# Optimization experiments

Hardware: AMD Instinct MI355X
Metric: run time of the kernel (lower is better)

The kernel has to match this reference:

```python
import jax, jax.numpy as jnp
import numpy as np

TEMPERATURE = 0.07
BALANCE = 1.0


def _l2norm(x, eps=1e-12):
    return x / jnp.maximum(jnp.linalg.norm(x, axis=1, keepdims=True), eps)


def setup_inputs() -> dict:
    key = jax.random.key(0)
    k1, k2 = jax.random.split(key)
    B, K, D = 32768, 8192, 384
    features = _l2norm(jax.random.normal(k1, (B, D), dtype=jnp.float32))
    centroids = jax.random.normal(k2, (K, D), dtype=jnp.float32)
    return {"features": features, "centroids": centroids}


def reference(features, centroids):
    # centroids: [K, D] learnable; features: [B, D] sampled batch (L2-normalized)
    c = _l2norm(centroids)
    # chunked matmul + exp + row-max in source == single fused GEMM+exp+max here
    prod_exp = jnp.exp(jnp.matmul(features, c.T) / TEMPERATURE)  # [B, K]
    pos_k = jnp.argmax(prod_exp, axis=1)                          # [B] int
    prod_exp_pos = jnp.max(prod_exp, axis=1)                      # [B]
    # centroid-centroid similarity; first operand is detached in source
    cent_exp = jnp.exp(jnp.matmul(jax.lax.stop_gradient(c), c.T) / TEMPERATURE)  # [K, K]
    cent_sum = jnp.sum(cent_exp, axis=0)                          # [K]
    J = jnp.log(prod_exp_pos) - jnp.log(prod_exp_pos + cent_sum[pos_k] * BALANCE)
    return -jnp.mean(J)
```

## Files before the change

### kernel.cpp

```cpp
#include <hip/hip_runtime.h>
#include <math.h>

constexpr int B = 32768;
constexpr int K = 8192;
constexpr int D = 384;
constexpr float INV_T = 1.0f / 0.07f;

constexpr int TILE_B = 24 * 64 * 16;

typedef int    int8v    __attribute__((ext_vector_type(8)));
typedef float  floatx16 __attribute__((ext_vector_type(16)));

__global__ __launch_bounds__(64) void normalize_k(const float* __restrict__ cent,
                                                  unsigned char* __restrict__ cbs) {
    const int row = blockIdx.x, lane = threadIdx.x;
    const float* src = cent + (size_t)row * D;
    float4 x = {0.f, 0.f, 0.f, 0.f}, y = {0.f, 0.f, 0.f, 0.f};
    if (lane < 48) {
        x = *(const float4*)(src + lane * 8);
        y = *(const float4*)(src + lane * 8 + 4);
    }
    float ss = x.x * x.x + x.y * x.y + x.z * x.z + x.w * x.w
             + y.x * y.x + y.y * y.y + y.z * y.z + y.w * y.w;
#pragma unroll
    for (int off = 32; off > 0; off >>= 1) ss += __shfl_down(ss, off, 64);
    ss = __shfl(ss, 0, 64);
    const float inv = 1.0f / fmaxf(sqrtf(ss), 1e-12f);
    if (lane < 48) {
        int w0 = __builtin_amdgcn_cvt_pk_fp8_f32(x.x * inv, x.y * inv, 0, false);
        w0 = __builtin_amdgcn_cvt_pk_fp8_f32(x.z * inv, x.w * inv, w0, true);
        int w1 = __builtin_amdgcn_cvt_pk_fp8_f32(y.x * inv, y.y * inv, 0, false);
        w1 = __builtin_amdgcn_cvt_pk_fp8_f32(y.z * inv, y.w * inv, w1, true);
        char* dst = (char*)cbs + (size_t)(row >> 6) * TILE_B
                  + ((size_t)(lane >> 1) * 64 + (row & 63)) * 16 + (lane & 1) * 8;
        *(int2*)dst = make_int2(w0, w1);
    }
}

__device__ __forceinline__ void stage_tile_async(const char* __restrict__ gtile,
                                                 char* __restrict__ bs,
                                                 int wave, int lane) {
    const char* g = gtile + wave * 6144 + lane * 16;
    char* l = bs + wave * 6144;
#pragma unroll
    for (int i = 0; i < 6; ++i) {
        __builtin_amdgcn_global_load_lds(
            (const __attribute__((address_space(1))) unsigned int*)(g + i * 1024),
            (__attribute__((address_space(3))) unsigned int*)(l + i * 1024),
            16, 0, 0);
    }
}

__device__ __forceinline__ int8v read_frag(const char* base, int t, int half) {
    const uint4 b0 = *(const uint4*)(base + (4 * t + 2 * half) * 1024);
    const uint4 b1 = *(const uint4*)(base + (4 * t + 2 * half + 1) * 1024);
    int8v f;
    f[0] = b0.x; f[1] = b0.y; f[2] = b0.z; f[3] = b0.w;
    f[4] = b1.x; f[5] = b1.y; f[6] = b1.z; f[7] = b1.w;
    return f;
}

__global__ __launch_bounds__(256, 3) void centsum_k(const unsigned char* __restrict__ cbs,
                                                    float* __restrict__ cent_sum) {
    __shared__ char bs[2][TILE_B];
    const int tid = threadIdx.x, lane = tid & 63, wave = tid >> 6;
    const int wm = wave >> 1, wn = wave & 1;
    const int l31 = lane & 31, half = lane >> 5;

    int8v afr[6];
    const char* abase = (const char*)cbs + (size_t)blockIdx.x * TILE_B
                      + (wm * 32 + l31) * 16;
#pragma unroll
    for (int t = 0; t < 6; ++t) afr[t] = read_frag(abase, t, half);

    float rs[16];
#pragma unroll
    for (int r = 0; r < 16; ++r) rs[r] = 0.f;

    const int ct0 = (blockIdx.x & 7) * 8;
    auto tile_of = [&](int it) { return blockIdx.y * 64 + ((ct0 + it) & 63); };

    stage_tile_async((const char*)cbs + (size_t)tile_of(0) * TILE_B, bs[0], wave, lane);
    int cur = 0;
    for (int it = 0; it < 64; ++it) {
        __syncthreads();
        if (it + 1 < 64)
            stage_tile_async((const char*)cbs + (size_t)tile_of(it + 1) * TILE_B,
                             bs[cur ^ 1], wave, lane);
        floatx16 acc;
#pragma unroll
        for (int r = 0; r < 16; ++r) acc[r] = 0.f;
        const char* bbase = bs[cur] + (wn * 32 + l31) * 16;
#pragma unroll
        for (int t = 0; t < 6; ++t) {
            const int8v bfr = read_frag(bbase, t, half);
            acc = __builtin_amdgcn_mfma_scale_f32_32x32x64_f8f6f4(
                      afr[t], bfr, acc, 0, 0, 0, 127, 0, 127);
        }
#pragma unroll
        for (int r = 0; r < 16; ++r) rs[r] += __expf(acc[r] * INV_T);
        cur ^= 1;
    }

#pragma unroll
    for (int r = 0; r < 16; ++r) {
        float s = rs[r];
#pragma unroll
        for (int off = 1; off < 32; off <<= 1) s += __shfl_xor(s, off, 64);
        if (l31 == 0) {
            const int rowl = (r & 3) + 8 * (r >> 2) + 4 * half;
            atomicAdd(&cent_sum[blockIdx.x * 64 + wm * 32 + rowl], s);
        }
    }
}

__global__ __launch_bounds__(256, 3) void rowmax_k(const float* __restrict__ f,
                                                   const unsigned char* __restrict__ cbs,
                                                   float* __restrict__ row_max,
                                                   int* __restrict__ row_arg) {
    __shared__ char bs[2][TILE_B];
    const int tid = threadIdx.x, lane = tid & 63, wave = tid >> 6;
    const int wm = wave >> 1, wn = wave & 1;
    const int l31 = lane & 31, half = lane >> 5;

    int8v afr[6];
    const float* arow = f + ((size_t)blockIdx.x * 64 + wm * 32 + l31) * D;
#pragma unroll
    for (int t = 0; t < 6; ++t) {
        const float* p = arow + t * 64 + half * 32;
        int8v a;
#pragma unroll
        for (int q = 0; q < 8; ++q) {
            const float4 v = *(const float4*)(p + q * 4);
            int w = __builtin_amdgcn_cvt_pk_fp8_f32(v.x, v.y, 0, false);
            w = __builtin_amdgcn_cvt_pk_fp8_f32(v.z, v.w, w, true);
            a[q] = w;
        }
        afr[t] = a;
    }

    float bestv[16];
    int   besti[16];
#pragma unroll
    for (int r = 0; r < 16; ++r) { bestv[r] = -INFINITY; besti[r] = 0; }

    const int ct0 = (blockIdx.x & 7) * 16;
    auto tile_of = [&](int it) { return (ct0 + it) & (K / 64 - 1); };

    stage_tile_async((const char*)cbs + (size_t)tile_of(0) * TILE_B, bs[0], wave, lane);
    int cur = 0;
    for (int it = 0; it < K / 64; ++it) {
        __syncthreads();
        if (it + 1 < K / 64)
            stage_tile_async((const char*)cbs + (size_t)tile_of(it + 1) * TILE_B,
                             bs[cur ^ 1], wave, lane);
        floatx16 acc;
#pragma unroll
        for (int r = 0; r < 16; ++r) acc[r] = 0.f;
        const char* bbase = bs[cur] + (wn * 32 + l31) * 16;
#pragma unroll
        for (int t = 0; t < 6; ++t) {
            const int8v bfr = read_frag(bbase, t, half);
            acc = __builtin_amdgcn_mfma_scale_f32_32x32x64_f8f6f4(
                      afr[t], bfr, acc, 0, 0, 0, 127, 0, 127);
        }
        const int curCol = tile_of(it) * 64 + wn * 32 + l31;
#pragma unroll
        for (int r = 0; r < 16; ++r) {
            const float v = acc[r];
            if (v > bestv[r]) { bestv[r] = v; besti[r] = curCol; }
        }
        cur ^= 1;
    }

#pragma unroll
    for (int r = 0; r < 16; ++r) {
        float v = bestv[r]; int ix = besti[r];
#pragma unroll
        for (int off = 1; off < 32; off <<= 1) {
            const float ov = __shfl_xor(v, off, 64);
            const int   oi = __shfl_xor(ix, off, 64);
            if (ov > v || (ov == v && oi < ix)) { v = ov; ix = oi; }
        }
        bestv[r] = v; besti[r] = ix;
    }

    __syncthreads();
    float* rv = (float*)bs;
    int*   ri = (int*)bs + 128;
    if (l31 == 0) {
#pragma unroll
        for (int r = 0; r < 16; ++r) {
            const int rowl = wm * 32 + (r & 3) + 8 * (r >> 2) + 4 * half;
            rv[rowl * 2 + wn] = bestv[r];
            ri[rowl * 2 + wn] = besti[r];
        }
    }
    __syncthreads();
    if (tid < 64) {
        const float v0 = rv[tid * 2], v1 = rv[tid * 2 + 1];
        const int   i0 = ri[tid * 2], i1 = ri[tid * 2 + 1];
        const bool take1 = (v1 > v0) || (v1 == v0 && i1 < i0);
        row_max[blockIdx.x * 64 + tid] = take1 ? v1 : v0;
        row_arg[blockIdx.x * 64 + tid] = take1 ? i1 : i0;
    }
}

__global__ __launch_bounds__(256) void loss_k(const float* __restrict__ row_max,
                                              const int* __restrict__ row_arg,
                                              const float* __restrict__ cent_sum,
                                              float* __restrict__ out) {
    __shared__ float red[256];
    const int tid = threadIdx.x;
    float s = 0.f;
    for (int b = blockIdx.x * 256 + tid; b < B; b += gridDim.x * 256) {
        const float m = row_max[b];
        const float cs = cent_sum[row_arg[b]];
        s += log1pf(cs * expf(-m * INV_T));
    }
    red[tid] = s;
    __syncthreads();
    for (int off = 128; off > 0; off >>= 1) {
        if (tid < off) red[tid] += red[tid + off];
        __syncthreads();
    }
    if (tid == 0) atomicAdd(out, red[0] / (float)B);
}

extern "C" void kernel_launch(void* const* d_in, const int* in_sizes, int n_in,
                              void* d_out, int out_size, void* d_ws, size_t ws_size,
                              hipStream_t stream) {
    const float* features  = (const float*)d_in[0];
    const float* centroids = (const float*)d_in[1];
    float* out = (float*)d_out;

    char* ws = (char*)d_ws;
    unsigned char* cbs = (unsigned char*)ws;
    float* cent_sum = (float*)(ws + (size_t)(K / 64) * TILE_B);
    float* row_max  = cent_sum + K;
    int*   row_arg  = (int*)(row_max + B);

    hipMemsetAsync(cent_sum, 0, K * sizeof(float), stream);
    hipMemsetAsync(out, 0, sizeof(float), stream);
    normalize_k<<<K, 64, 0, stream>>>(centroids, cbs);
    centsum_k<<<dim3(K / 64, 2), 256, 0, stream>>>(cbs, cent_sum);
    rowmax_k<<<B / 64, 256, 0, stream>>>(features, cbs, row_max, row_arg);
    loss_k<<<64, 256, 0, stream>>>(row_max, row_arg, cent_sum, out);
}
```

Measured before the change: 278.6 us.

## Double per-wave row tile and split column range across blocks in GEMM kernels

After: 235.4 us. 15.5% less time.

```diff
diff --git a/kernel.cpp b/kernel.cpp
--- a/kernel.cpp
+++ b/kernel.cpp
@@ -60,163 +60,193 @@
     return f;
 }
 
-__global__ __launch_bounds__(256, 3) void centsum_k(const unsigned char* __restrict__ cbs,
+__global__ __launch_bounds__(256, 2) void centsum_k(const unsigned char* __restrict__ cbs,
                                                     float* __restrict__ cent_sum) {
     __shared__ char bs[2][TILE_B];
     const int tid = threadIdx.x, lane = tid & 63, wave = tid >> 6;
     const int wm = wave >> 1, wn = wave & 1;
     const int l31 = lane & 31, half = lane >> 5;
-
-    int8v afr[6];
-    const char* abase = (const char*)cbs + (size_t)blockIdx.x * TILE_B
-                      + (wm * 32 + l31) * 16;
-#pragma unroll
-    for (int t = 0; t < 6; ++t) afr[t] = read_frag(abase, t, half);
-
-    float rs[16];
-#pragma unroll
-    for (int r = 0; r < 16; ++r) rs[r] = 0.f;
-
-    const int ct0 = (blockIdx.x & 7) * 8;
-    auto tile_of = [&](int it) { return blockIdx.y * 64 + ((ct0 + it) & 63); };
+    const int rb = blockIdx.x >> 3, ch = blockIdx.x & 7;
+
+    const int stag = (rb & 3) * 4;
+    auto tile_of = [&](int it) { return ch * 16 + ((stag + it) & 15); };
 
     stage_tile_async((const char*)cbs + (size_t)tile_of(0) * TILE_B, bs[0], wave, lane);
+
+    int8v afr[2][6];
+#pragma unroll
+    for (int s = 0; s < 2; ++s) {
+        const char* abase = (const char*)cbs + (size_t)(rb * 2 + wm) * TILE_B
+                          + (s * 32 + l31) * 16;
+#pragma unroll
+        for (int t = 0; t < 6; ++t) afr[s][t] = read_frag(abase, t, half);
+    }
+
+    float rs[2][16];
+#pragma unroll
+    for (int s = 0; s < 2; ++s)
+#pragma unroll
+        for (int r = 0; r < 16; ++r) rs[s][r] = 0.f;
+
+    int cur = 0;
+    for (int it = 0; it < 16; ++it) {
+        __syncthreads();
+        if (it + 1 < 16)
+            stage_tile_async((const char*)cbs + (size_t)tile_of(it + 1) * TILE_B,
+                             bs[cur ^ 1], wave, lane);
+        floatx16 acc0, acc1;
+#pragma unroll
+        for (int r = 0; r < 16; ++r) { acc0[r] = 0.f; acc1[r] = 0.f; }
+        const char* bbase = bs[cur] + (wn * 32 + l31) * 16;
+#pragma unroll
+        for (int t = 0; t < 6; ++t) {
+            const int8v bfr = read_frag(bbase, t, half);
+            acc0 = __builtin_amdgcn_mfma_scale_f32_32x32x64_f8f6f4(
+                       afr[0][t], bfr, acc0, 0, 0, 0, 127, 0, 127);
+            acc1 = __builtin_amdgcn_mfma_scale_f32_32x32x64_f8f6f4(
+                       afr[1][t], bfr, acc1, 0, 0, 0, 127, 0, 127);
+        }
+#pragma unroll
+        for (int r = 0; r < 16; ++r) {
+            rs[0][r] += __expf(acc0[r] * INV_T);
+            rs[1][r] += __expf(acc1[r] * INV_T);
+        }
+        cur ^= 1;
+    }
+
+#pragma unroll
+    for (int s = 0; s < 2; ++s)
+#pragma unroll
+        for (int r = 0; r < 16; ++r) {
+            float v = rs[s][r];
+#pragma unroll
+            for (int off = 1; off < 32; off <<= 1) v += __shfl_xor(v, off, 64);
+            if (l31 == 0) {
+                const int rowl = (r & 3) + 8 * (r >> 2) + 4 * half;
+                atomicAdd(&cent_sum[rb * 128 + wm * 64 + s * 32 + rowl], v);
+            }
+        }
+}
+
+__global__ __launch_bounds__(256, 2) void rowmax_k(const float* __restrict__ f,
+                                                   const unsigned char* __restrict__ cbs,
+                                                   float* __restrict__ row_max2,
+                                                   int* __restrict__ row_arg2) {
+    __shared__ char bs[2][TILE_B];
+    const int tid = threadIdx.x, lane = tid & 63, wave = tid >> 6;
+    const int wm = wave >> 1, wn = wave & 1;
+    const int l31 = lane & 31, half = lane >> 5;
+    const int rb = blockIdx.x >> 1, ch = blockIdx.x & 1;
+
+    const int stag = (rb & 7) * 8;
+    auto tile_of = [&](int it) { return ch * 64 + ((stag + it) & 63); };
+
+    stage_tile_async((const char*)cbs + (size_t)tile_of(0) * TILE_B, bs[0], wave, lane);
+
+    int8v afr[2][6];
+    const int rowbase = rb * 128 + wm * 64;
+#pragma unroll
+    for (int s = 0; s < 2; ++s) {
+        const float* arow = f + (size_t)(rowbase + s * 32 + l31) * D;
+#pragma unroll
+        for (int t = 0; t < 6; ++t) {
+            const float* p = arow + t * 64 + half * 32;
+            int8v a;
+#pragma unroll
+            for (int q = 0; q < 8; ++q) {
+                const float4 v = *(const float4*)(p + q * 4);
+                int w = __builtin_amdgcn_cvt_pk_fp8_f32(v.x, v.y, 0, false);
+                w = __builtin_amdgcn_cvt_pk_fp8_f32(v.z, v.w, w, true);
+                a[q] = w;
+            }
+            afr[s][t] = a;
+        }
+    }
+
+    float bv[2][16];
+    int   bi[2][16];
+#pragma unroll
+    for (int s = 0; s < 2; ++s)
+#pragma unroll
+        for (int r = 0; r < 16; ++r) { bv[s][r] = -INFINITY; bi[s][r] = 0; }
+
     int cur = 0;
     for (int it = 0; it < 64; ++it) {
         __syncthreads();
         if (it + 1 < 64)
             stage_tile_async((const char*)cbs + (size_t)tile_of(it + 1) * TILE_B,
                              bs[cur ^ 1], wave, lane);
-        floatx16 acc;
-#pragma unroll
-        for (int r = 0; r < 16; ++r) acc[r] = 0.f;
+        floatx16 acc0, acc1;
+#pragma unroll
+        for (int r = 0; r < 16; ++r) { acc0[r] = 0.f; acc1[r] = 0.f; }
         const char* bbase = bs[cur] + (wn * 32 + l31) * 16;
 #pragma unroll
         for (int t = 0; t < 6; ++t) {
             const int8v bfr = read_frag(bbase, t, half);
-            acc = __builtin_amdgcn_mfma_scale_f32_32x32x64_f8f6f4(
-                      afr[t], bfr, acc, 0, 0, 0, 127, 0, 127);
-        }
-#pragma unroll
-        for (int r = 0; r < 16; ++r) rs[r] += __expf(acc[r] * INV_T);
+            acc0 = __builtin_amdgcn_mfma_scale_f32_32x32x64_f8f6f4(
+                       afr[0][t], bfr, acc0, 0, 0, 0, 127, 0, 127);
+            acc1 = __builtin_amdgcn_mfma_scale_f32_32x32x64_f8f6f4(
+                       afr[1][t], bfr, acc1, 0, 0, 0, 127, 0, 127);
+        }
+        const int curCol = tile_of(it) * 64 + wn * 32 + l31;
+#pragma unroll
+        for (int r = 0; r < 16; ++r) {
+            if (acc0[r] > bv[0][r]) { bv[0][r] = acc0[r]; bi[0][r] = curCol; }
+            if (acc1[r] > bv[1][r]) { bv[1][r] = acc1[r]; bi[1][r] = curCol; }
+        }
         cur ^= 1;
     }
 
 #pragma unroll
-    for (int r = 0; r < 16; ++r) {
-        float s = rs[r];
-#pragma unroll
-        for (int off = 1; off < 32; off <<= 1) s += __shfl_xor(s, off, 64);
-        if (l31 == 0) {
-            const int rowl = (r & 3) + 8 * (r >> 2) + 4 * half;
-            atomicAdd(&cent_sum[blockIdx.x * 64 + wm * 32 + rowl], s);
-        }
-    }
-}
-
-__global__ __launch_bounds__(256, 3) void rowmax_k(const float* __restrict__ f,
-                                                   const unsigned char* __restrict__ cbs,
-                                                   float* __restrict__ row_max,
-                                                   int* __restrict__ row_arg) {
-    __shared__ char bs[2][TILE_B];
-    const int tid = threadIdx.x, lane = tid & 63, wave = tid >> 6;
-    const int wm = wave >> 1, wn = wave & 1;
-    const int l31 = lane & 31, half = lane >> 5;
-
-    int8v afr[6];
-    const float* arow = f + ((size_t)blockIdx.x * 64 + wm * 32 + l31) * D;
-#pragma unroll
-    for (int t = 0; t < 6; ++t) {
-        const float* p = arow + t * 64 + half * 32;
-        int8v a;
-#pragma unroll
-        for (int q = 0; q < 8; ++q) {
-            const float4 v = *(const float4*)(p + q * 4);
-            int w = __builtin_amdgcn_cvt_pk_fp8_f32(v.x, v.y, 0, false);
-            w = __builtin_amdgcn_cvt_pk_fp8_f32(v.z, v.w, w, true);
-            a[q] = w;
-        }
-        afr[t] = a;
-    }
-
-    float bestv[16];
-    int   besti[16];
-#pragma unroll
-    for (int r = 0; r < 16; ++r) { bestv[r] = -INFINITY; besti[r] = 0; }
-
-    const int ct0 = (blockIdx.x & 7) * 16;
-    auto tile_of = [&](int it) { return (ct0 + it) & (K / 64 - 1); };
-
-    stage_tile_async((const char*)cbs + (size_t)tile_of(0) * TILE_B, bs[0], wave, lane);
-    int cur = 0;
-    for (int it = 0; it < K / 64; ++it) {
-        __syncthreads();
-        if (it + 1 < K / 64)
-            stage_tile_async((const char*)cbs + (size_t)tile_of(it + 1) * TILE_B,
-                             bs[cur ^ 1], wave, lane);
-        floatx16 acc;
-#pragma unroll
-        for (int r = 0; r < 16; ++r) acc[r] = 0.f;
-        const char* bbase = bs[cur] + (wn * 32 + l31) * 16;
-#pragma unroll
-        for (int t = 0; t < 6; ++t) {
-            const int8v bfr = read_frag(bbase, t, half);
-            acc = __builtin_amdgcn_mfma_scale_f32_32x32x64_f8f6f4(
-                      afr[t], bfr, acc, 0, 0, 0, 127, 0, 127);
-        }
-        const int curCol = tile_of(it) * 64 + wn * 32 + l31;
-#pragma unroll
-        for (int r = 0; r < 16; ++r) {
-            const float v = acc[r];
-            if (v > bestv[r]) { bestv[r] = v; besti[r] = curCol; }
-        }
-        cur ^= 1;
-    }
-
-#pragma unroll
-    for (int r = 0; r < 16; ++r) {
-        float v = bestv[r]; int ix = besti[r];
-#pragma unroll
-        for (int off = 1; off < 32; off <<= 1) {
-            const float ov = __shfl_xor(v, off, 64);
-            const int   oi = __shfl_xor(ix, off, 64);
-            if (ov > v || (ov == v && oi < ix)) { v = ov; ix = oi; }
-        }
-        bestv[r] = v; besti[r] = ix;
-    }
+    for (int s = 0; s < 2; ++s)
+#pragma unroll
+        for (int r = 0; r < 16; ++r) {
+            float v = bv[s][r]; int ix = bi[s][r];
+#pragma unroll
+            for (int off = 1; off < 32; off <<= 1) {
+                const float ov = __shfl_xor(v, off, 64);
+                const int   oi = __shfl_xor(ix, off, 64);
+                if (ov > v || (ov == v && oi < ix)) { v = ov; ix = oi; }
+            }
+            bv[s][r] = v; bi[s][r] = ix;
+        }
 
     __syncthreads();
     float* rv = (float*)bs;
-    int*   ri = (int*)bs + 128;
+    int*   ri = (int*)bs + 256;
     if (l31 == 0) {
 #pragma unroll
-        for (int r = 0; r < 16; ++r) {
-            const int rowl = wm * 32 + (r & 3) + 8 * (r >> 2) + 4 * half;
-            rv[rowl * 2 + wn] = bestv[r];
-            ri[rowl * 2 + wn] = besti[r];
-        }
+        for (int s = 0; s < 2; ++s)
+#pragma unroll
+            for (int r = 0; r < 16; ++r) {
+                const int row = wm * 64 + s * 32 + (r & 3) + 8 * (r >> 2) + 4 * half;
+                rv[row * 2 + wn] = bv[s][r];
+                ri[row * 2 + wn] = bi[s][r];
+            }
     }
     __syncthreads();
-    if (tid < 64) {
+    if (tid < 128) {
         const float v0 = rv[tid * 2], v1 = rv[tid * 2 + 1];
         const int   i0 = ri[tid * 2], i1 = ri[tid * 2 + 1];
         const bool take1 = (v1 > v0) || (v1 == v0 && i1 < i0);
-        row_max[blockIdx.x * 64 + tid] = take1 ? v1 : v0;
-        row_arg[blockIdx.x * 64 + tid] = take1 ? i1 : i0;
-    }
-}
-
-__global__ __launch_bounds__(256) void loss_k(const float* __restrict__ row_max,
-                                              const int* __restrict__ row_arg,
+        row_max2[(size_t)(rb * 128 + tid) * 2 + ch] = take1 ? v1 : v0;
+        row_arg2[(size_t)(rb * 128 + tid) * 2 + ch] = take1 ? i1 : i0;
+    }
+}
+
+__global__ __launch_bounds__(256) void loss_k(const float* __restrict__ row_max2,
+                                              const int* __restrict__ row_arg2,
                                               const float* __restrict__ cent_sum,
                                               float* __restrict__ out) {
     __shared__ float red[256];
     const int tid = threadIdx.x;
     float s = 0.f;
     for (int b = blockIdx.x * 256 + tid; b < B; b += gridDim.x * 256) {
-        const float m = row_max[b];
-        const float cs = cent_sum[row_arg[b]];
-        s += log1pf(cs * expf(-m * INV_T));
+        const float m0 = row_max2[(size_t)b * 2], m1 = row_max2[(size_t)b * 2 + 1];
+        const bool take1 = m1 > m0;
+        const float m = take1 ? m1 : m0;
+        const int ix = row_arg2[(size_t)b * 2 + (take1 ? 1 : 0)];
+        s += log1pf(cent_sum[ix] * expf(-m * INV_T));
     }
     red[tid] = s;
     __syncthreads();
@@ -237,13 +267,13 @@
     char* ws = (char*)d_ws;
     unsigned char* cbs = (unsigned char*)ws;
     float* cent_sum = (float*)(ws + (size_t)(K / 64) * TILE_B);
-    float* row_max  = cent_sum + K;
-    int*   row_arg  = (int*)(row_max + B);
+    float* row_max2 = cent_sum + K;
+    int*   row_arg2 = (int*)(row_max2 + 2 * B);
 
     hipMemsetAsync(cent_sum, 0, K * sizeof(float), stream);
     hipMemsetAsync(out, 0, sizeof(float), stream);
     normalize_k<<<K, 64, 0, stream>>>(centroids, cbs);
-    centsum_k<<<dim3(K / 64, 2), 256, 0, stream>>>(cbs, cent_sum);
-    rowmax_k<<<B / 64, 256, 0, stream>>>(features, cbs, row_max, row_arg);
-    loss_k<<<64, 256, 0, stream>>>(row_max, row_arg, cent_sum, out);
-}
+    centsum_k<<<(K / 128) * 8, 256, 0, stream>>>(cbs, cent_sum);
+    rowmax_k<<<(B / 128) * 2, 256, 0, stream>>>(features, cbs, row_max2, row_arg2);
+    loss_k<<<64, 256, 0, stream>>>(row_max2, row_arg2, cent_sum, out);
+}
```
